# Performance work log

Measured on AMD Instinct MI355X. Metric: run time of the kernel, lower is better.

## Reference

```python
import jax, jax.numpy as jnp
import numpy as np

EPS = 1e-5
DN = ('NCHW', 'OIHW', 'NCHW')

def _conv(x, w):
    return jax.lax.conv_general_dilated(x, w, (1, 1), 'VALID', dimension_numbers=DN)

def _bn4(x, g, b, m, v):
    # BatchNorm2d in eval mode, per-channel over NCHW
    inv = g / jnp.sqrt(v + EPS)
    return x * inv[None, :, None, None] + (b - m * inv)[None, :, None, None]

def _bn1(x, g, b, m, v):
    inv = g / jnp.sqrt(v + EPS)
    return x * inv[None, :] + (b - m * inv)[None, :]

def _hardtanh(x):
    return jnp.clip(x, -1.0, 1.0)

def _sign(x):
    return jnp.sign(x)

def _maxpool2(x):
    return jax.lax.reduce_window(x, -jnp.inf, jax.lax.max,
                                 (1, 1, 2, 2), (1, 1, 2, 2), 'VALID')

def setup_inputs() -> dict:
    key = jax.random.key(0)
    ks = jax.random.split(key, 20)
    B = 8192
    d = {
        'x': jax.random.normal(ks[0], (B, 8, 16, 16), jnp.float32),
        'w0': jax.random.normal(ks[1], (32, 8, 3, 3), jnp.float32) * 0.1,
        'b0': jax.random.normal(ks[2], (32,), jnp.float32) * 0.1,
        'g1': jax.random.uniform(ks[3], (32,), jnp.float32, 0.5, 1.5),
        'be1': jax.random.normal(ks[4], (32,), jnp.float32) * 0.1,
        'm1': jax.random.normal(ks[5], (32,), jnp.float32) * 0.1,
        'v1': jax.random.uniform(ks[6], (32,), jnp.float32, 0.5, 1.5),
        'w2': jax.random.normal(ks[7], (32, 32, 3, 3), jnp.float32) * 0.1,
        'g2': jax.random.uniform(ks[8], (32,), jnp.float32, 0.5, 1.5),
        'be2': jax.random.normal(ks[9], (32,), jnp.float32) * 0.1,
        'm2': jax.random.normal(ks[10], (32,), jnp.float32) * 0.1,
        'v2': jax.random.uniform(ks[11], (32,), jnp.float32, 0.5, 1.5),
        'w_fc': jax.random.normal(ks[12], (516, 1152), jnp.float32) * 0.03,
        'g3': jax.random.uniform(ks[13], (516,), jnp.float32, 0.5, 1.5),
        'be3': jax.random.normal(ks[14], (516,), jnp.float32) * 0.1,
        'm3': jax.random.normal(ks[15], (516,), jnp.float32) * 0.1,
        'v3': jax.random.uniform(ks[16], (516,), jnp.float32, 0.5, 1.5),
        'w_last': jax.random.normal(ks[17], (10, 516), jnp.float32) * 0.05,
        'b_last': jax.random.normal(ks[18], (10,), jnp.float32) * 0.05,
    }
    return d

def reference(x, w0, b0, g1, be1, m1, v1, w2, g2, be2, m2, v2,
              w_fc, g3, be3, m3, v3, w_last, b_last):
    # initial float conv + BN + Hardtanh
    h = _conv(x, w0) + b0[None, :, None, None]          # [B,32,14,14]
    h = _hardtanh(_bn4(h, g1, be1, m1, v1))
    # binarized conv (sign(input), sign(weight), no bias)
    h = _conv(_sign(h), _sign(w2))                      # [B,32,12,12]
    h = _hardtanh(_bn4(h, g2, be2, m2, v2))
    h = _maxpool2(h)                                    # [B,32,6,6]
    # dropout is identity in eval mode
    h = h.reshape(h.shape[0], -1)                       # [B,1152]
    # binarized linear (no bias)
    h = _sign(h) @ _sign(w_fc).T                        # [B,516]
    h = _hardtanh(_bn1(h, g3, be3, m3, v3))
    return h @ w_last.T + b_last[None, :]               # [B,10]
```

## Files before the change

kernel.cpp:

```cpp
#include <hip/hip_runtime.h>
#include <cstdint>

#define EPSF 1e-5f

typedef __attribute__((ext_vector_type(8))) short short8;
typedef __attribute__((ext_vector_type(4))) float f32x4;
typedef __attribute__((ext_vector_type(4))) unsigned int u32x4;

__device__ inline uint32_t bf16rne(float x) {
    uint32_t u = __builtin_bit_cast(uint32_t, x);
    return (u + 0x7fffu + ((u >> 16) & 1u)) >> 16;
}
__device__ inline float bf16f(uint32_t b) {
    return __builtin_bit_cast(float, b << 16);
}

__global__ __launch_bounds__(256) void prep_kernel(
    const float* __restrict__ w2, const float* __restrict__ wfc,
    const float* __restrict__ g3, const float* __restrict__ be3,
    const float* __restrict__ m3, const float* __restrict__ v3,
    const float* __restrict__ wlast,
    const float* __restrict__ w0, const float* __restrict__ b0,
    const float* __restrict__ g1, const float* __restrict__ be1,
    const float* __restrict__ m1, const float* __restrict__ v1,
    uint32_t* __restrict__ w2bits, uint32_t* __restrict__ wfcb,
    float* __restrict__ inv3p, float* __restrict__ sh3p, float* __restrict__ wlt,
    uint32_t* __restrict__ bfrag, float2* __restrict__ bn1c)
{
    const int tid = threadIdx.x;
    if (blockIdx.x < 129) {
        const int wid = tid >> 6, lane = tid & 63;
        const int j = blockIdx.x * 4 + wid;
        const int c = lane & 31, pp = lane >> 5;
        const float* row = wfc + j * 1152 + c * 36;
        #pragma unroll
        for (int i = 0; i < 18; i++) {
            int pos = 2 * i + pp;
            float v = row[pos];
            unsigned long long mb = __ballot(v < 0.f);
            if (lane == 0)  wfcb[(2 * i) * 576 + j]     = (uint32_t)mb;
            if (lane == 32) wfcb[(2 * i + 1) * 576 + j] = (uint32_t)(mb >> 32);
        }
        return;
    }
    int id = (blockIdx.x - 129) * 256 + tid;
    if (id < 288) {
        int co = id / 9, r = id % 9;
        uint32_t b = 0;
        for (int ci = 0; ci < 32; ci++)
            b |= (uint32_t)(w2[(co * 32 + ci) * 9 + r] < 0.f) << ci;
        w2bits[id] = b;
        return;
    }
    id -= 288;
    if (id < 576) {
        float iv = 0.f, sh = 0.f;
        if (id < 516) {
            iv = g3[id] / sqrtf(__fadd_rn(v3[id], EPSF));
            sh = __fsub_rn(be3[id], __fmul_rn(m3[id], iv));
        }
        inv3p[id] = iv; sh3p[id] = sh;
        return;
    }
    id -= 576;
    if (id < 5760) {
        int k = id / 576, j = id % 576;
        wlt[id] = (j < 516) ? wlast[k * 516 + j] : 0.f;
        return;
    }
    id -= 5760;
    if (id < 768) {
        int L = id / 12, r = id % 12;
        int nt = r / 6, s = (r % 6) / 2, h = r & 1;
        int g = L >> 4, n = L & 15;
        int tap = 4 * s + g;
        uint32_t d[4] = {0, 0, 0, 0};
        if (tap < 9) {
            int co = nt * 16 + n;
            for (int j2 = 0; j2 < 4; j2++) {
                float wa = w0[co * 72 + (2 * j2) * 9 + tap];
                float wb = w0[co * 72 + (2 * j2 + 1) * 9 + tap];
                uint32_t ha = bf16rne(wa), hb = bf16rne(wb);
                uint32_t va, vb;
                if (h == 0) { va = ha; vb = hb; }
                else { va = bf16rne(wa - bf16f(ha)); vb = bf16rne(wb - bf16f(hb)); }
                d[j2] = va | (vb << 16);
            }
        }
        *(u32x4*)(bfrag + id * 4) = (u32x4){d[0], d[1], d[2], d[3]};
        return;
    }
    id -= 768;
    if (id < 32) {
        float iv = g1[id] / sqrtf(__fadd_rn(v1[id], EPSF));
        float sh = __fsub_rn(be1[id], __fmul_rn(m1[id], iv));
        float off = __fadd_rn(__fmul_rn(b0[id], iv), sh);
        bn1c[id] = make_float2(iv, off);
        return;
    }
    id -= 32;
    if (id < 2160) {
        int p = id / 60, j = 516 + id % 60;
        wfcb[p * 576 + j] = 0u;
    }
}

__device__ __noinline__ bool recheck_sign(const float* __restrict__ xim,
                                          const float* __restrict__ w0,
                                          int py, int px, int co,
                                          float ivc, float offc)
{
    double ad = 0.0;
    for (int ci = 0; ci < 8; ci++)
        for (int ky = 0; ky < 3; ky++)
            for (int kx = 0; kx < 3; kx++)
                ad = fma((double)xim[ci * 256 + (py + ky) * 16 + px + kx],
                         (double)w0[co * 72 + ci * 9 + ky * 3 + kx], ad);
    return (ad * (double)ivc + (double)offc) < 0.0;
}

__global__ __launch_bounds__(256, 4) void convA(
    const float* __restrict__ x, const float* __restrict__ w0,
    const uint32_t* __restrict__ bfrag, const float2* __restrict__ bn1c,
    uint32_t* __restrict__ s1bits)
{
    __shared__ __align__(16) char simg[2][9216];

    const int t = threadIdx.x;
    const int wv = t >> 6, lane = t & 63;
    const int ilocal = wv >> 1;
    const int w01 = wv & 1;
    const int img = blockIdx.x * 2 + ilocal;
    const float* xim = x + img * 2048;
    char* hib = simg[ilocal];
    char* lob = simg[ilocal] + 4608;

    const int g = lane >> 4;
    const int n = lane & 15;

    short8 Bh[2][3], Bl[2][3];
    {
        const uint32_t* bb = bfrag + lane * 48;
        #pragma unroll
        for (int nt = 0; nt < 2; nt++)
            #pragma unroll
            for (int s = 0; s < 3; s++) {
                Bh[nt][s] = *(const short8*)(bb + (nt * 6 + s * 2) * 4);
                Bl[nt][s] = *(const short8*)(bb + (nt * 6 + s * 2 + 1) * 4);
            }
    }
    const float2 bnA = bn1c[n], bnB = bn1c[16 + n];

    #pragma unroll
    for (int q = 0; q < 2; q++) {
        int pos = w01 * 128 + 64 * q + lane;
        float v[8];
        #pragma unroll
        for (int ci = 0; ci < 8; ci++) v[ci] = xim[ci * 256 + pos];
        uint32_t hw[4], lw[4];
        #pragma unroll
        for (int j2 = 0; j2 < 4; j2++) {
            float a = v[2 * j2], b = v[2 * j2 + 1];
            uint32_t ha = bf16rne(a), hb = bf16rne(b);
            uint32_t la = bf16rne(a - bf16f(ha)), lb = bf16rne(b - bf16f(hb));
            hw[j2] = ha | (hb << 16);
            lw[j2] = la | (lb << 16);
        }
        *(u32x4*)(hib + pos * 16) = (u32x4){hw[0], hw[1], hw[2], hw[3]};
        *(u32x4*)(lob + pos * 16) = (u32x4){lw[0], lw[1], lw[2], lw[3]};
    }
    if (w01 == 1 && lane < 32) {
        *(u32x4*)(hib + (256 + lane) * 16) = (u32x4){0, 0, 0, 0};
        *(u32x4*)(lob + (256 + lane) * 16) = (u32x4){0, 0, 0, 0};
    }

    int koff[3];
    #pragma unroll
    for (int s = 0; s < 3; s++) {
        int tap = 4 * s + g;
        koff[s] = (tap < 9) ? ((tap / 3) * 16 + (tap % 3)) * 16 : 0;
    }

    __syncthreads();

    uint32_t* outb = s1bits + img * 196;
    const int tstart = w01 ? 7 : 0, tend = w01 ? 13 : 7;

    for (int tile = tstart; tile < tend; ++tile) {
        int posA = tile * 16 + n;
        int pyA = posA / 14, pxA = posA - pyA * 14;
        int sl = (pyA * 16 + pxA) * 16;

        f32x4 acc0 = {0.f, 0.f, 0.f, 0.f}, acc1 = {0.f, 0.f, 0.f, 0.f};
        #pragma unroll
        for (int s = 0; s < 3; s++) {
            short8 Ah = *(const short8*)(hib + sl + koff[s]);
            short8 Al = *(const short8*)(lob + sl + koff[s]);
            acc0 = __builtin_amdgcn_mfma_f32_16x16x32_bf16(Al, Bh[0][s], acc0, 0, 0, 0);
            acc0 = __builtin_amdgcn_mfma_f32_16x16x32_bf16(Ah, Bl[0][s], acc0, 0, 0, 0);
            acc0 = __builtin_amdgcn_mfma_f32_16x16x32_bf16(Ah, Bh[0][s], acc0, 0, 0, 0);
            acc1 = __builtin_amdgcn_mfma_f32_16x16x32_bf16(Al, Bh[1][s], acc1, 0, 0, 0);
            acc1 = __builtin_amdgcn_mfma_f32_16x16x32_bf16(Ah, Bl[1][s], acc1, 0, 0, 0);
            acc1 = __builtin_amdgcn_mfma_f32_16x16x32_bf16(Ah, Bh[1][s], acc1, 0, 0, 0);
        }

        #pragma unroll
        for (int r = 0; r < 4; r++) {
            int pos = tile * 16 + 4 * g + r;
            float yv0 = fmaf(acc0[r], bnA.x, bnA.y);
            float yv1 = fmaf(acc1[r], bnB.x, bnB.y);
            bool bit0, bit1;
            if (__builtin_expect(pos < 196 && fabsf(yv0) < 3e-4f, 0)) {
                int py = pos / 14, px = pos - py * 14;
                bit0 = recheck_sign(xim, w0, py, px, n, bnA.x, bnA.y);
            } else bit0 = (yv0 < 0.f);
            if (__builtin_expect(pos < 196 && fabsf(yv1) < 3e-4f, 0)) {
                int py = pos / 14, px = pos - py * 14;
                bit1 = recheck_sign(xim, w0, py, px, 16 + n, bnB.x, bnB.y);
            } else bit1 = (yv1 < 0.f);
            unsigned long long m0 = __ballot(bit0);
            unsigned long long m1 = __ballot(bit1);
            uint32_t word = (uint32_t)((m0 >> (16 * g)) & 0xffffull)
                          | ((uint32_t)((m1 >> (16 * g)) & 0xffffull) << 16);
            if (n == 0 && pos < 196) outb[pos] = word;
        }
    }
}

__global__ __launch_bounds__(256) void convBF(
    const uint32_t* __restrict__ s1bits, const uint32_t* __restrict__ w2bits,
    const float* __restrict__ g2, const float* __restrict__ be2,
    const float* __restrict__ m2, const float* __restrict__ v2,
    const uint32_t* __restrict__ wfcb,
    const float* __restrict__ inv3p, const float* __restrict__ sh3p,
    const float* __restrict__ wlt, const float* __restrict__ blast,
    float* __restrict__ out)
{
    __shared__ uint32_t s1l[8][196];
    __shared__ uint32_t l_in[288];
    const int t = threadIdx.x, wid = t >> 6, lane = t & 63;

    for (int i = t; i < 1568; i += 256)
        ((uint32_t*)s1l)[i] = s1bits[blockIdx.x * 1568 + i];

    const int c = lane & 31, h = lane >> 5;
    uint32_t wr[9];
    #pragma unroll
    for (int k = 0; k < 9; k++) wr[k] = w2bits[c * 9 + k];
    float ivv = g2[c] / sqrtf(__fadd_rn(v2[c], EPSF));
    float shv = __fsub_rn(be2[c], __fmul_rn(m2[c], ivv));
    __syncthreads();

    for (int rep = 0; rep < 2; rep++) {
        const int iml = wid * 2 + rep;
        const uint32_t* s1w = s1l[iml];
        uint32_t* outp = &l_in[iml * 36];

        for (int yy = 0; yy < 3; yy++) {
            const int y2 = yy + 3 * h;
            const int rbase = 2 * y2 * 14;
            uint32_t win[4][4];
            #pragma unroll
            for (int rr = 0; rr < 4; rr++) {
                uint2 a = *(const uint2*)&s1w[rbase + rr * 14];
                uint2 b = *(const uint2*)&s1w[rbase + rr * 14 + 2];
                win[rr][0] = a.x; win[rr][1] = a.y; win[rr][2] = b.x; win[rr][3] = b.y;
            }
            for (int x2 = 0; x2 < 6; x2++) {
                if (x2 > 0) {
                    #pragma unroll
                    for (int rr = 0; rr < 4; rr++) {
                        win[rr][0] = win[rr][2]; win[rr][1] = win[rr][3];
                        uint2 b = *(const uint2*)&s1w[rbase + rr * 14 + 2 * x2 + 2];
                        win[rr][2] = b.x; win[rr][3] = b.y;
                    }
                }
                int mx = -10000;
                #pragma unroll
                for (int dy = 0; dy < 2; dy++)
                    #pragma unroll
                    for (int dx = 0; dx < 2; dx++) {
                        int p = 0;
                        #pragma unroll
                        for (int ky = 0; ky < 3; ky++)
                            #pragma unroll
                            for (int kx = 0; kx < 3; kx++)
                                p += __popc(win[dy + ky][dx + kx] ^ wr[ky * 3 + kx]);
                        mx = max(mx, 288 - 2 * p);
                    }
                float yv = __fadd_rn(__fmul_rn((float)mx, ivv), shv);
                unsigned long long mb = __ballot(yv < 0.f);
                int pos = y2 * 6 + x2;
                if (lane == 0)  outp[pos] = (uint32_t)mb;
                if (lane == 32) outp[pos] = (uint32_t)(mb >> 32);
            }
        }
    }
    __syncthreads();

    const int b0i = blockIdx.x * 8 + wid * 2;
    const uint32_t* in0 = &l_in[wid * 72];

    int pc0[9], pc1[9];
    #pragma unroll
    for (int q = 0; q < 9; q++) { pc0[q] = 0; pc1[q] = 0; }

    for (int w = 0; w < 36; w++) {
        uint32_t i0 = in0[w], i1 = in0[36 + w];
        const uint32_t* wf = wfcb + w * 576 + lane;
        #pragma unroll
        for (int q = 0; q < 9; q++) {
            uint32_t f = wf[q * 64];
            pc0[q] += __popc(i0 ^ f);
            pc1[q] += __popc(i1 ^ f);
        }
    }

    float oa[2][10];
    #pragma unroll
    for (int b = 0; b < 2; b++)
        #pragma unroll
        for (int k = 0; k < 10; k++) oa[b][k] = 0.f;

    #pragma unroll
    for (int q = 0; q < 9; q++) {
        int j = lane + 64 * q;
        float iv3 = inv3p[j], sh3 = sh3p[j];
        float t0 = fminf(1.f, fmaxf(-1.f, __fadd_rn(__fmul_rn((float)(1152 - 2 * pc0[q]), iv3), sh3)));
        float t1 = fminf(1.f, fmaxf(-1.f, __fadd_rn(__fmul_rn((float)(1152 - 2 * pc1[q]), iv3), sh3)));
        #pragma unroll
        for (int k = 0; k < 10; k++) {
            float wvv = wlt[k * 576 + j];
            oa[0][k] = fmaf(t0, wvv, oa[0][k]);
            oa[1][k] = fmaf(t1, wvv, oa[1][k]);
        }
    }

    #pragma unroll
    for (int m = 1; m < 64; m <<= 1)
        #pragma unroll
        for (int b = 0; b < 2; b++)
            #pragma unroll
            for (int k = 0; k < 10; k++)
                oa[b][k] += __shfl_xor(oa[b][k], m, 64);

    if (lane == 0) {
        for (int b = 0; b < 2; b++)
            for (int k = 0; k < 10; k++)
                out[(b0i + b) * 10 + k] = oa[b][k] + blast[k];
    }
}

extern "C" void kernel_launch(void* const* d_in, const int* in_sizes, int n_in,
                              void* d_out, int out_size, void* d_ws, size_t ws_size,
                              hipStream_t stream)
{
    (void)in_sizes; (void)n_in; (void)out_size; (void)ws_size;
    const float* x     = (const float*)d_in[0];
    const float* w0    = (const float*)d_in[1];
    const float* b0    = (const float*)d_in[2];
    const float* g1    = (const float*)d_in[3];
    const float* be1   = (const float*)d_in[4];
    const float* m1    = (const float*)d_in[5];
    const float* v1    = (const float*)d_in[6];
    const float* w2    = (const float*)d_in[7];
    const float* g2    = (const float*)d_in[8];
    const float* be2   = (const float*)d_in[9];
    const float* m2    = (const float*)d_in[10];
    const float* v2    = (const float*)d_in[11];
    const float* wfc   = (const float*)d_in[12];
    const float* g3    = (const float*)d_in[13];
    const float* be3   = (const float*)d_in[14];
    const float* m3    = (const float*)d_in[15];
    const float* v3    = (const float*)d_in[16];
    const float* wlast = (const float*)d_in[17];
    const float* blast = (const float*)d_in[18];

    char* ws = (char*)d_ws;
    uint32_t* s1bits = (uint32_t*)(ws);
    uint32_t* w2bits = (uint32_t*)(ws + 6422528);
    uint32_t* wfcb   = (uint32_t*)(ws + 6423680);
    float*    inv3p  = (float*)(ws + 6506624);
    float*    sh3p   = (float*)(ws + 6508928);
    float*    wlt    = (float*)(ws + 6511232);
    uint32_t* bfrag  = (uint32_t*)(ws + 6534272);
    float2*   bn1c   = (float2*)(ws + 6546560);

    prep_kernel<<<167, 256, 0, stream>>>(w2, wfc, g3, be3, m3, v3, wlast,
                                         w0, b0, g1, be1, m1, v1,
                                         w2bits, wfcb, inv3p, sh3p, wlt,
                                         bfrag, bn1c);
    convA<<<4096, 256, 0, stream>>>(x, w0, bfrag, bn1c, s1bits);
    convBF<<<1024, 256, 0, stream>>>(s1bits, w2bits, g2, be2, m2, v2,
                                     wfcb, inv3p, sh3p, wlt, blast, (float*)d_out);
}
```

Before: 226.6 us.

## Fuse weight prep into convA and process two images per wave

Drops the separate prep kernel. The first conv's bf16 weight fragments and BN1 constants are now built per block in LDS, and the remaining weight preprocessing runs in extra trailing blocks of the same launch. Each wave now owns two whole images in sequence, prefetching the second image's input into registers with vector loads while the first is converted, which cuts the grid from 4096 to 1188 blocks. This saves one launch and overlaps global loads with conversion, at the cost of redundant per-block fragment building and fewer, longer-running blocks.

```diff
diff --git a/kernel.cpp b/kernel.cpp
--- a/kernel.cpp
+++ b/kernel.cpp
@@ -13,96 +13,6 @@
 }
 __device__ inline float bf16f(uint32_t b) {
     return __builtin_bit_cast(float, b << 16);
-}
-
-__global__ __launch_bounds__(256) void prep_kernel(
-    const float* __restrict__ w2, const float* __restrict__ wfc,
-    const float* __restrict__ g3, const float* __restrict__ be3,
-    const float* __restrict__ m3, const float* __restrict__ v3,
-    const float* __restrict__ wlast,
-    const float* __restrict__ w0, const float* __restrict__ b0,
-    const float* __restrict__ g1, const float* __restrict__ be1,
-    const float* __restrict__ m1, const float* __restrict__ v1,
-    uint32_t* __restrict__ w2bits, uint32_t* __restrict__ wfcb,
-    float* __restrict__ inv3p, float* __restrict__ sh3p, float* __restrict__ wlt,
-    uint32_t* __restrict__ bfrag, float2* __restrict__ bn1c)
-{
-    const int tid = threadIdx.x;
-    if (blockIdx.x < 129) {
-        const int wid = tid >> 6, lane = tid & 63;
-        const int j = blockIdx.x * 4 + wid;
-        const int c = lane & 31, pp = lane >> 5;
-        const float* row = wfc + j * 1152 + c * 36;
-        #pragma unroll
-        for (int i = 0; i < 18; i++) {
-            int pos = 2 * i + pp;
-            float v = row[pos];
-            unsigned long long mb = __ballot(v < 0.f);
-            if (lane == 0)  wfcb[(2 * i) * 576 + j]     = (uint32_t)mb;
-            if (lane == 32) wfcb[(2 * i + 1) * 576 + j] = (uint32_t)(mb >> 32);
-        }
-        return;
-    }
-    int id = (blockIdx.x - 129) * 256 + tid;
-    if (id < 288) {
-        int co = id / 9, r = id % 9;
-        uint32_t b = 0;
-        for (int ci = 0; ci < 32; ci++)
-            b |= (uint32_t)(w2[(co * 32 + ci) * 9 + r] < 0.f) << ci;
-        w2bits[id] = b;
-        return;
-    }
-    id -= 288;
-    if (id < 576) {
-        float iv = 0.f, sh = 0.f;
-        if (id < 516) {
-            iv = g3[id] / sqrtf(__fadd_rn(v3[id], EPSF));
-            sh = __fsub_rn(be3[id], __fmul_rn(m3[id], iv));
-        }
-        inv3p[id] = iv; sh3p[id] = sh;
-        return;
-    }
-    id -= 576;
-    if (id < 5760) {
-        int k = id / 576, j = id % 576;
-        wlt[id] = (j < 516) ? wlast[k * 516 + j] : 0.f;
-        return;
-    }
-    id -= 5760;
-    if (id < 768) {
-        int L = id / 12, r = id % 12;
-        int nt = r / 6, s = (r % 6) / 2, h = r & 1;
-        int g = L >> 4, n = L & 15;
-        int tap = 4 * s + g;
-        uint32_t d[4] = {0, 0, 0, 0};
-        if (tap < 9) {
-            int co = nt * 16 + n;
-            for (int j2 = 0; j2 < 4; j2++) {
-                float wa = w0[co * 72 + (2 * j2) * 9 + tap];
-                float wb = w0[co * 72 + (2 * j2 + 1) * 9 + tap];
-                uint32_t ha = bf16rne(wa), hb = bf16rne(wb);
-                uint32_t va, vb;
-                if (h == 0) { va = ha; vb = hb; }
-                else { va = bf16rne(wa - bf16f(ha)); vb = bf16rne(wb - bf16f(hb)); }
-                d[j2] = va | (vb << 16);
-            }
-        }
-        *(u32x4*)(bfrag + id * 4) = (u32x4){d[0], d[1], d[2], d[3]};
-        return;
-    }
-    id -= 768;
-    if (id < 32) {
-        float iv = g1[id] / sqrtf(__fadd_rn(v1[id], EPSF));
-        float sh = __fsub_rn(be1[id], __fmul_rn(m1[id], iv));
-        float off = __fadd_rn(__fmul_rn(b0[id], iv), sh);
-        bn1c[id] = make_float2(iv, off);
-        return;
-    }
-    id -= 32;
-    if (id < 2160) {
-        int p = id / 60, j = 516 + id % 60;
-        wfcb[p * 576 + j] = 0u;
-    }
 }
 
 __device__ __noinline__ bool recheck_sign(const float* __restrict__ xim,
@@ -119,28 +29,109 @@
     return (ad * (double)ivc + (double)offc) < 0.0;
 }
 
-__global__ __launch_bounds__(256, 4) void convA(
+__global__ __launch_bounds__(256, 4) void convAP(
     const float* __restrict__ x, const float* __restrict__ w0,
-    const uint32_t* __restrict__ bfrag, const float2* __restrict__ bn1c,
-    uint32_t* __restrict__ s1bits)
+    const float* __restrict__ b0, const float* __restrict__ g1,
+    const float* __restrict__ be1, const float* __restrict__ m1,
+    const float* __restrict__ v1,
+    const float* __restrict__ w2, const float* __restrict__ wfc,
+    const float* __restrict__ g3, const float* __restrict__ be3,
+    const float* __restrict__ m3, const float* __restrict__ v3,
+    const float* __restrict__ wlast,
+    uint32_t* __restrict__ s1bits, uint32_t* __restrict__ w2bits,
+    uint32_t* __restrict__ wfcb, float* __restrict__ inv3p,
+    float* __restrict__ sh3p, float* __restrict__ wlt)
 {
-    __shared__ __align__(16) char simg[2][9216];
-
+    __shared__ __align__(16) char lds[4][9216];
     const int t = threadIdx.x;
+
+    if (blockIdx.x >= 1024) {
+        int pb = blockIdx.x - 1024;
+        if (pb < 129) {
+            const int wid = t >> 6, lane2 = t & 63;
+            const int j = pb * 4 + wid;
+            const int c = lane2 & 31, pp = lane2 >> 5;
+            const float* row = wfc + j * 1152 + c * 36;
+            #pragma unroll
+            for (int i = 0; i < 18; i++) {
+                int pos = 2 * i + pp;
+                float v = row[pos];
+                unsigned long long mb = __ballot(v < 0.f);
+                if (lane2 == 0)  wfcb[(2 * i) * 576 + j]     = (uint32_t)mb;
+                if (lane2 == 32) wfcb[(2 * i + 1) * 576 + j] = (uint32_t)(mb >> 32);
+            }
+            return;
+        }
+        int id = (pb - 129) * 256 + t;
+        if (id < 288) {
+            int co = id / 9, r = id % 9;
+            uint32_t b = 0;
+            for (int ci = 0; ci < 32; ci++)
+                b |= (uint32_t)(w2[(co * 32 + ci) * 9 + r] < 0.f) << ci;
+            w2bits[id] = b;
+            return;
+        }
+        id -= 288;
+        if (id < 576) {
+            float iv = 0.f, sh = 0.f;
+            if (id < 516) {
+                iv = g3[id] / sqrtf(__fadd_rn(v3[id], EPSF));
+                sh = __fsub_rn(be3[id], __fmul_rn(m3[id], iv));
+            }
+            inv3p[id] = iv; sh3p[id] = sh;
+            return;
+        }
+        id -= 576;
+        if (id < 5760) {
+            int k = id / 576, j = id % 576;
+            wlt[id] = (j < 516) ? wlast[k * 516 + j] : 0.f;
+            return;
+        }
+        id -= 5760;
+        if (id < 2160) {
+            int p = id / 60, j = 516 + id % 60;
+            wfcb[p * 576 + j] = 0u;
+        }
+        return;
+    }
+
     const int wv = t >> 6, lane = t & 63;
-    const int ilocal = wv >> 1;
-    const int w01 = wv & 1;
-    const int img = blockIdx.x * 2 + ilocal;
-    const float* xim = x + img * 2048;
-    char* hib = simg[ilocal];
-    char* lob = simg[ilocal] + 4608;
-
-    const int g = lane >> 4;
-    const int n = lane & 15;
+    const int g = lane >> 4, n = lane & 15;
+
+    uint32_t* bfl = (uint32_t*)&lds[0][0];
+    float2*   bnl = (float2*)(&lds[0][0] + 12288);
+
+    for (int e = t; e < 768; e += 256) {
+        int L = e / 12, r = e % 12;
+        int nt = r / 6, s = (r % 6) / 2, h = r & 1;
+        int gg = L >> 4, nn = L & 15;
+        int tap = 4 * s + gg;
+        uint32_t d[4] = {0, 0, 0, 0};
+        if (tap < 9) {
+            int co = nt * 16 + nn;
+            #pragma unroll
+            for (int j2 = 0; j2 < 4; j2++) {
+                float wa = w0[co * 72 + (2 * j2) * 9 + tap];
+                float wb = w0[co * 72 + (2 * j2 + 1) * 9 + tap];
+                uint32_t ha = bf16rne(wa), hb = bf16rne(wb);
+                uint32_t va, vb;
+                if (h == 0) { va = ha; vb = hb; }
+                else { va = bf16rne(wa - bf16f(ha)); vb = bf16rne(wb - bf16f(hb)); }
+                d[j2] = va | (vb << 16);
+            }
+        }
+        *(u32x4*)(bfl + e * 4) = (u32x4){d[0], d[1], d[2], d[3]};
+    }
+    if (t < 32) {
+        float iv = g1[t] / sqrtf(__fadd_rn(v1[t], EPSF));
+        float sh = __fsub_rn(be1[t], __fmul_rn(m1[t], iv));
+        bnl[t] = make_float2(iv, __fadd_rn(__fmul_rn(b0[t], iv), sh));
+    }
+    __syncthreads();
 
     short8 Bh[2][3], Bl[2][3];
     {
-        const uint32_t* bb = bfrag + lane * 48;
+        const uint32_t* bb = bfl + lane * 48;
         #pragma unroll
         for (int nt = 0; nt < 2; nt++)
             #pragma unroll
@@ -149,27 +140,13 @@
                 Bl[nt][s] = *(const short8*)(bb + (nt * 6 + s * 2 + 1) * 4);
             }
     }
-    const float2 bnA = bn1c[n], bnB = bn1c[16 + n];
-
-    #pragma unroll
-    for (int q = 0; q < 2; q++) {
-        int pos = w01 * 128 + 64 * q + lane;
-        float v[8];
-        #pragma unroll
-        for (int ci = 0; ci < 8; ci++) v[ci] = xim[ci * 256 + pos];
-        uint32_t hw[4], lw[4];
-        #pragma unroll
-        for (int j2 = 0; j2 < 4; j2++) {
-            float a = v[2 * j2], b = v[2 * j2 + 1];
-            uint32_t ha = bf16rne(a), hb = bf16rne(b);
-            uint32_t la = bf16rne(a - bf16f(ha)), lb = bf16rne(b - bf16f(hb));
-            hw[j2] = ha | (hb << 16);
-            lw[j2] = la | (lb << 16);
-        }
-        *(u32x4*)(hib + pos * 16) = (u32x4){hw[0], hw[1], hw[2], hw[3]};
-        *(u32x4*)(lob + pos * 16) = (u32x4){lw[0], lw[1], lw[2], lw[3]};
-    }
-    if (w01 == 1 && lane < 32) {
+    const float2 bnA = bnl[n], bnB = bnl[16 + n];
+    __syncthreads();
+
+    char* hib = lds[wv];
+    char* lob = lds[wv] + 4608;
+
+    if (lane < 32) {
         *(u32x4*)(hib + (256 + lane) * 16) = (u32x4){0, 0, 0, 0};
         *(u32x4*)(lob + (256 + lane) * 16) = (u32x4){0, 0, 0, 0};
     }
@@ -181,48 +158,81 @@
         koff[s] = (tap < 9) ? ((tap / 3) * 16 + (tap % 3)) * 16 : 0;
     }
 
-    __syncthreads();
-
-    uint32_t* outb = s1bits + img * 196;
-    const int tstart = w01 ? 7 : 0, tend = w01 ? 13 : 7;
-
-    for (int tile = tstart; tile < tend; ++tile) {
-        int posA = tile * 16 + n;
-        int pyA = posA / 14, pxA = posA - pyA * 14;
-        int sl = (pyA * 16 + pxA) * 16;
-
-        f32x4 acc0 = {0.f, 0.f, 0.f, 0.f}, acc1 = {0.f, 0.f, 0.f, 0.f};
-        #pragma unroll
-        for (int s = 0; s < 3; s++) {
-            short8 Ah = *(const short8*)(hib + sl + koff[s]);
-            short8 Al = *(const short8*)(lob + sl + koff[s]);
-            acc0 = __builtin_amdgcn_mfma_f32_16x16x32_bf16(Al, Bh[0][s], acc0, 0, 0, 0);
-            acc0 = __builtin_amdgcn_mfma_f32_16x16x32_bf16(Ah, Bl[0][s], acc0, 0, 0, 0);
-            acc0 = __builtin_amdgcn_mfma_f32_16x16x32_bf16(Ah, Bh[0][s], acc0, 0, 0, 0);
-            acc1 = __builtin_amdgcn_mfma_f32_16x16x32_bf16(Al, Bh[1][s], acc1, 0, 0, 0);
-            acc1 = __builtin_amdgcn_mfma_f32_16x16x32_bf16(Ah, Bl[1][s], acc1, 0, 0, 0);
-            acc1 = __builtin_amdgcn_mfma_f32_16x16x32_bf16(Ah, Bh[1][s], acc1, 0, 0, 0);
-        }
-
-        #pragma unroll
-        for (int r = 0; r < 4; r++) {
-            int pos = tile * 16 + 4 * g + r;
-            float yv0 = fmaf(acc0[r], bnA.x, bnA.y);
-            float yv1 = fmaf(acc1[r], bnB.x, bnB.y);
-            bool bit0, bit1;
-            if (__builtin_expect(pos < 196 && fabsf(yv0) < 3e-4f, 0)) {
-                int py = pos / 14, px = pos - py * 14;
-                bit0 = recheck_sign(xim, w0, py, px, n, bnA.x, bnA.y);
-            } else bit0 = (yv0 < 0.f);
-            if (__builtin_expect(pos < 196 && fabsf(yv1) < 3e-4f, 0)) {
-                int py = pos / 14, px = pos - py * 14;
-                bit1 = recheck_sign(xim, w0, py, px, 16 + n, bnB.x, bnB.y);
-            } else bit1 = (yv1 < 0.f);
-            unsigned long long m0 = __ballot(bit0);
-            unsigned long long m1 = __ballot(bit1);
-            uint32_t word = (uint32_t)((m0 >> (16 * g)) & 0xffffull)
-                          | ((uint32_t)((m1 >> (16 * g)) & 0xffffull) << 16);
-            if (n == 0 && pos < 196) outb[pos] = word;
+    const int imgbase = blockIdx.x * 8 + wv * 2;
+
+    f32x4 pf[8];
+    {
+        const float* xb = x + (size_t)imgbase * 2048 + lane * 4;
+        #pragma unroll
+        for (int ci = 0; ci < 8; ci++) pf[ci] = *(const f32x4*)(xb + ci * 256);
+    }
+
+    for (int it = 0; it < 2; it++) {
+        const int img = imgbase + it;
+        const float* xim = x + (size_t)img * 2048;
+
+        #pragma unroll
+        for (int e = 0; e < 4; e++) {
+            int p = 4 * lane + e;
+            uint32_t hw[4], lw[4];
+            #pragma unroll
+            for (int j2 = 0; j2 < 4; j2++) {
+                float a  = pf[2 * j2][e];
+                float bv = pf[2 * j2 + 1][e];
+                uint32_t ha = bf16rne(a), hb = bf16rne(bv);
+                uint32_t la = bf16rne(a - bf16f(ha)), lb = bf16rne(bv - bf16f(hb));
+                hw[j2] = ha | (hb << 16);
+                lw[j2] = la | (lb << 16);
+            }
+            *(u32x4*)(hib + p * 16) = (u32x4){hw[0], hw[1], hw[2], hw[3]};
+            *(u32x4*)(lob + p * 16) = (u32x4){lw[0], lw[1], lw[2], lw[3]};
+        }
+
+        if (it == 0) {
+            const float* xb1 = x + (size_t)(imgbase + 1) * 2048 + lane * 4;
+            #pragma unroll
+            for (int ci = 0; ci < 8; ci++) pf[ci] = *(const f32x4*)(xb1 + ci * 256);
+        }
+
+        uint32_t* outb = s1bits + (size_t)img * 196;
+        for (int tile = 0; tile < 13; ++tile) {
+            int posA = tile * 16 + n;
+            int pyA = posA / 14, pxA = posA - pyA * 14;
+            int sl = (pyA * 16 + pxA) * 16;
+
+            f32x4 acc0 = {0.f, 0.f, 0.f, 0.f}, acc1 = {0.f, 0.f, 0.f, 0.f};
+            #pragma unroll
+            for (int s = 0; s < 3; s++) {
+                short8 Ah = *(const short8*)(hib + sl + koff[s]);
+                short8 Al = *(const short8*)(lob + sl + koff[s]);
+                acc0 = __builtin_amdgcn_mfma_f32_16x16x32_bf16(Al, Bh[0][s], acc0, 0, 0, 0);
+                acc0 = __builtin_amdgcn_mfma_f32_16x16x32_bf16(Ah, Bl[0][s], acc0, 0, 0, 0);
+                acc0 = __builtin_amdgcn_mfma_f32_16x16x32_bf16(Ah, Bh[0][s], acc0, 0, 0, 0);
+                acc1 = __builtin_amdgcn_mfma_f32_16x16x32_bf16(Al, Bh[1][s], acc1, 0, 0, 0);
+                acc1 = __builtin_amdgcn_mfma_f32_16x16x32_bf16(Ah, Bl[1][s], acc1, 0, 0, 0);
+                acc1 = __builtin_amdgcn_mfma_f32_16x16x32_bf16(Ah, Bh[1][s], acc1, 0, 0, 0);
+            }
+
+            #pragma unroll
+            for (int r = 0; r < 4; r++) {
+                int pos = tile * 16 + 4 * g + r;
+                float yv0 = fmaf(acc0[r], bnA.x, bnA.y);
+                float yv1 = fmaf(acc1[r], bnB.x, bnB.y);
+                bool bit0, bit1;
+                if (__builtin_expect(pos < 196 && fabsf(yv0) < 3e-4f, 0)) {
+                    int py = pos / 14, px = pos - py * 14;
+                    bit0 = recheck_sign(xim, w0, py, px, n, bnA.x, bnA.y);
+                } else bit0 = (yv0 < 0.f);
+                if (__builtin_expect(pos < 196 && fabsf(yv1) < 3e-4f, 0)) {
+                    int py = pos / 14, px = pos - py * 14;
+                    bit1 = recheck_sign(xim, w0, py, px, 16 + n, bnB.x, bnB.y);
+                } else bit1 = (yv1 < 0.f);
+                unsigned long long m0 = __ballot(bit0);
+                unsigned long long m1 = __ballot(bit1);
+                uint32_t word = (uint32_t)((m0 >> (16 * g)) & 0xffffull)
+                              | ((uint32_t)((m1 >> (16 * g)) & 0xffffull) << 16);
+                if (n == 0 && pos < 196) outb[pos] = word;
+            }
         }
     }
 }
@@ -383,14 +393,10 @@
     float*    inv3p  = (float*)(ws + 6506624);
     float*    sh3p   = (float*)(ws + 6508928);
     float*    wlt    = (float*)(ws + 6511232);
-    uint32_t* bfrag  = (uint32_t*)(ws + 6534272);
-    float2*   bn1c   = (float2*)(ws + 6546560);
-
-    prep_kernel<<<167, 256, 0, stream>>>(w2, wfc, g3, be3, m3, v3, wlast,
-                                         w0, b0, g1, be1, m1, v1,
-                                         w2bits, wfcb, inv3p, sh3p, wlt,
-                                         bfrag, bn1c);
-    convA<<<4096, 256, 0, stream>>>(x, w0, bfrag, bn1c, s1bits);
+
+    convAP<<<1188, 256, 0, stream>>>(x, w0, b0, g1, be1, m1, v1,
+                                     w2, wfc, g3, be3, m3, v3, wlast,
+                                     s1bits, w2bits, wfcb, inv3p, sh3p, wlt);
     convBF<<<1024, 256, 0, stream>>>(s1bits, w2bits, g2, be2, m2, v2,
                                      wfcb, inv3p, sh3p, wlt, blast, (float*)d_out);
 }
```

Result: slower. 240.7 us (+6.2%).
